# Kernel tuning notes

Measured on AMD Instinct MI355X. Metric: run time of the kernel, lower is better.

Reference implementation:

```python
import jax, jax.numpy as jnp
import numpy as np

# fixed-point config (matches init_kwargs)
DIM, H = 768, 12
DHEAD = DIM // H
DATA_W, DATA_F = 32, 16        # input activation quantizer
WQ = WK = WV = WP = (16, 8)    # weight quantizers (width, frac)
BQ = BK = BV = BP = (16, 8)    # bias quantizers
DQ = DK = DV = DS = DZ = (16, 8)  # activation quantizers after each stage
OUT_W, OUT_F = 32, 8


def qfix(x, width, frac):
    """Fixed-point integer quantizer: round to 2^-frac grid, clamp to signed width."""
    scale = jnp.float32(2.0 ** frac)
    lo = -(2.0 ** (width - 1))
    hi = 2.0 ** (width - 1) - 1
    return jnp.clip(jnp.round(x * scale), lo, hi) / scale


def setup_inputs() -> dict:
    key = jax.random.key(0)
    ks = jax.random.split(key, 5)
    return {
        "q_in": jax.random.normal(ks[0], (2, 2048, DIM), dtype=jnp.float32),
        "wqkv": jax.random.normal(ks[1], (3 * DIM, DIM), dtype=jnp.float32) * 0.05,
        "bqkv": jax.random.normal(ks[2], (3 * DIM,), dtype=jnp.float32) * 0.05,
        "wp": jax.random.normal(ks[3], (DIM, DIM), dtype=jnp.float32) * 0.05,
        "bp": jax.random.normal(ks[4], (DIM,), dtype=jnp.float32) * 0.05,
    }


def reference(q_in, wqkv, bqkv, wp, bp):
    B, N, _ = q_in.shape
    # per-head weight split: wqkv -> (H, 3*DHEAD, DIM), rows [0:d]=q, [d:2d]=k, [2d:3d]=v
    w = wqkv.reshape(H, 3 * DHEAD, DIM)
    b = bqkv.reshape(H, 3 * DHEAD)
    wq_, wk_, wv_ = w[:, :DHEAD], w[:, DHEAD:2 * DHEAD], w[:, 2 * DHEAD:]
    bq_, bk_, bv_ = b[:, :DHEAD], b[:, DHEAD:2 * DHEAD], b[:, 2 * DHEAD:]

    x = qfix(q_in, DATA_W, DATA_F)  # QuantizedLinear input quantization

    def qlin(wt, bt, wcfg, bcfg, ocfg):
        # y[b,h,n,e] = x[b,n,d] @ qw[h,e,d]^T + qb[h,e], then output quantize
        y = jnp.einsum('bnd,hed->bhne', x, qfix(wt, *wcfg)) + qfix(bt, *bcfg)[None, :, None, :]
        return qfix(y, *ocfg)

    q = qlin(wq_, bq_, WQ, BQ, DQ)  # (B,H,N,DHEAD)
    k = qlin(wk_, bk_, WK, BK, DK)
    v = qlin(wv_, bv_, WV, BV, DV)

    s = qfix(jnp.einsum('bhne,bhme->bhnm', q, k), *DS)   # (B,H,N,N) quantized scores
    z = qfix(jnp.einsum('bhnm,bhme->bhne', s, v), *DZ)   # (B,H,N,DHEAD)

    # concat heads along feature dim (torch.cat dim=2)
    zc = z.transpose(0, 2, 1, 3).reshape(B, N, DIM)

    # quantized projection: input quantized with data_z cfg (idempotent here)
    out = jnp.einsum('bnd,ed->bne', qfix(zc, *DZ), qfix(wp, *WP)) + qfix(bp, *BP)
    return qfix(out, OUT_W, OUT_F)
```

## Files before the change

### kernel.cpp

```cpp
#include <hip/hip_runtime.h>


#define NTOK 4096
#define DIM  768
#define NH   12
#define DH   64
#define SEQ  2048
#define QKVD 2304
#define NBH  24
#define LSTR 72

typedef _Float16 half8 __attribute__((ext_vector_type(8)));
typedef _Float16 half4 __attribute__((ext_vector_type(4)));
typedef __fp16   fp16x2 __attribute__((ext_vector_type(2)));
typedef float floatx4 __attribute__((ext_vector_type(4)));
typedef float floatx16 __attribute__((ext_vector_type(16)));

__global__ __launch_bounds__(256) void prep(
    const float* __restrict__ X,
    const float* __restrict__ wqkv, const float* __restrict__ bqkv,
    const float* __restrict__ wp,   const float* __restrict__ bp,
    _Float16* __restrict__ Xh, _Float16* __restrict__ Xl,
    _Float16* __restrict__ W16, _Float16* __restrict__ Wp16,
    float* __restrict__ bq24, float* __restrict__ bp16)
{
    int i = blockIdx.x * 256 + threadIdx.x;
    int i4 = i * 4;
    if (i4 < NTOK * DIM) {
        float4 x = *(const float4*)(X + i4);
        float xi[4] = {x.x, x.y, x.z, x.w};
        half4 oh, ol;
#pragma unroll
        for (int j = 0; j < 4; ++j) {
            float v = rintf(xi[j] * 65536.0f);
            float h = rintf(v * (1.0f / 2048.0f));
            ((_Float16*)&oh)[j] = (_Float16)h;
            ((_Float16*)&ol)[j] = (_Float16)(v - 2048.0f * h);
        }
        *(half4*)(Xh + i4) = oh;
        *(half4*)(Xl + i4) = ol;
    }
    if (i4 < QKVD * DIM) {
        float4 w = *(const float4*)(wqkv + i4);
        half4 o = {(_Float16)rintf(w.x * 256.0f), (_Float16)rintf(w.y * 256.0f),
                   (_Float16)rintf(w.z * 256.0f), (_Float16)rintf(w.w * 256.0f)};
        *(half4*)(W16 + i4) = o;
    }
    if (i4 < DIM * DIM) {
        float4 w = *(const float4*)(wp + i4);
        half4 o = {(_Float16)rintf(w.x * 256.0f), (_Float16)rintf(w.y * 256.0f),
                   (_Float16)rintf(w.z * 256.0f), (_Float16)rintf(w.w * 256.0f)};
        *(half4*)(Wp16 + i4) = o;
    }
    if (i < QKVD) bq24[i] = rintf(bqkv[i] * 256.0f) * 65536.0f;
    if (i < DIM)  bp16[i] = rintf(bp[i] * 256.0f) * 256.0f;
}

__global__ __launch_bounds__(256) void qkv_mfma(
    const _Float16* __restrict__ Xh, const _Float16* __restrict__ Xl,
    const _Float16* __restrict__ W16, const float* __restrict__ bq24,
    _Float16* __restrict__ Q16, _Float16* __restrict__ K16,
    _Float16* __restrict__ Vt16)
{
    __shared__ __align__(16) _Float16 Ah[64 * LSTR];
    __shared__ __align__(16) _Float16 Al[64 * LSTR];
    __shared__ __align__(16) _Float16 Bs[128 * LSTR];
    const int t = threadIdx.x;
    const int wave = t >> 6, lane = t & 63;
    const int lrow = lane & 15, quad = lane >> 4;
    const int m0 = blockIdx.y * 64;
    const int col0 = blockIdx.x * 128;

    floatx4 acch[4][2], accl[4][2];
#pragma unroll
    for (int fm = 0; fm < 4; ++fm)
#pragma unroll
        for (int fn = 0; fn < 2; ++fn) {
            acch[fm][fn] = (floatx4){0.f, 0.f, 0.f, 0.f};
            accl[fm][fn] = (floatx4){0.f, 0.f, 0.f, 0.f};
        }

    for (int k0 = 0; k0 < DIM; k0 += 64) {
        __syncthreads();
#pragma unroll
        for (int i = 0; i < 2; ++i) {
            int id = t + 256 * i;
            int r = id >> 3, c8 = id & 7;
            *(half8*)(&Ah[r * LSTR + c8 * 8]) =
                *(const half8*)(Xh + (size_t)(m0 + r) * DIM + k0 + c8 * 8);
            *(half8*)(&Al[r * LSTR + c8 * 8]) =
                *(const half8*)(Xl + (size_t)(m0 + r) * DIM + k0 + c8 * 8);
        }
#pragma unroll
        for (int i = 0; i < 4; ++i) {
            int id = t + 256 * i;
            int r = id >> 3, c8 = id & 7;
            *(half8*)(&Bs[r * LSTR + c8 * 8]) =
                *(const half8*)(W16 + (size_t)(col0 + r) * DIM + k0 + c8 * 8);
        }
        __syncthreads();
#pragma unroll
        for (int kk = 0; kk < 64; kk += 32) {
            half8 bf[2];
#pragma unroll
            for (int fn = 0; fn < 2; ++fn)
                bf[fn] = *(const half8*)(&Bs[(wave * 32 + fn * 16 + lrow) * LSTR + kk + quad * 8]);
#pragma unroll
            for (int fm = 0; fm < 4; ++fm) {
                half8 ah = *(const half8*)(&Ah[(fm * 16 + lrow) * LSTR + kk + quad * 8]);
                half8 al = *(const half8*)(&Al[(fm * 16 + lrow) * LSTR + kk + quad * 8]);
#pragma unroll
                for (int fn = 0; fn < 2; ++fn) {
                    acch[fm][fn] = __builtin_amdgcn_mfma_f32_16x16x32_f16(ah, bf[fn], acch[fm][fn], 0, 0, 0);
                    accl[fm][fn] = __builtin_amdgcn_mfma_f32_16x16x32_f16(al, bf[fn], accl[fm][fn], 0, 0, 0);
                }
            }
        }
    }

    const int b_ = m0 >> 11;
    const int n0base = m0 & 2047;
#pragma unroll
    for (int fn = 0; fn < 2; ++fn) {
        const int c = col0 + wave * 32 + fn * 16 + lrow;
        const int h = c / 192;
        const int jj = c % 192;
        const int kind = jj >> 6;
        const int e = jj & 63;
        const int bh = b_ * NH + h;
        const float bb = bq24[c];
#pragma unroll
        for (int fm = 0; fm < 4; ++fm) {
            float qv[4];
#pragma unroll
            for (int rg = 0; rg < 4; ++rg) {
                float y = fmaf(2048.0f, acch[fm][fn][rg], accl[fm][fn][rg]) + bb;
                float q = rintf(y * (1.0f / 65536.0f));
                qv[rg] = fminf(fmaxf(q, -32768.0f), 32767.0f);
            }
            if (kind == 2) {
                const int n0v = n0base + fm * 16 + 8 * (quad & 1) + 4 * (quad >> 1);
                half4 o = {(_Float16)qv[0], (_Float16)qv[1], (_Float16)qv[2], (_Float16)qv[3]};
                *(half4*)(Vt16 + ((size_t)bh * DH + e) * SEQ + n0v) = o;
            } else {
                const int n0 = n0base + fm * 16 + quad * 4;
                _Float16* dst = (kind == 0) ? Q16 : K16;
#pragma unroll
                for (int rg = 0; rg < 4; ++rg)
                    dst[((size_t)bh * SEQ + n0 + rg) * DH + e] = (_Float16)qv[rg];
            }
        }
    }
}

__global__ __launch_bounds__(256, 3) void attention_mfma(
    const _Float16* __restrict__ Q16, const _Float16* __restrict__ K16,
    const _Float16* __restrict__ Vt16,
    _Float16* __restrict__ Zh16, _Float16* __restrict__ Zl16)
{
    __shared__ __align__(16) char smem[64 * LSTR * 2 * 2];
    _Float16* Ks = (_Float16*)smem;
    _Float16* Vs = Ks + 64 * LSTR;
    float* scr = (float*)smem;

    const int t = threadIdx.x;
    const int bh = blockIdx.x;
    const int qt = blockIdx.y;
    const int w = t >> 6, lane = t & 63;
    const int l31 = lane & 31, hi = lane >> 5;
    const int wj = w & 1;
    const int wi = w >> 1;
    const _Float16* Qg = Q16 + ((size_t)bh * SEQ + qt * 64) * DH;
    const _Float16* Kg = K16 + (size_t)bh * SEQ * DH;
    const _Float16* Vg = Vt16 + (size_t)bh * DH * SEQ;

    half8 qf[4];
#pragma unroll
    for (int i = 0; i < 4; ++i)
        qf[i] = *(const half8*)(Qg + (32 * wj + l31) * DH + 16 * i + 8 * hi);

    floatx16 acc0h, acc0l, acc1h, acc1l;
#pragma unroll
    for (int r = 0; r < 16; ++r) { acc0h[r] = 0.f; acc0l[r] = 0.f; acc1h[r] = 0.f; acc1l[r] = 0.f; }

    for (int m0 = 0; m0 < SEQ; m0 += 64) {
        __syncthreads();
        {
            int r = t >> 3, k8 = t & 7;
            *(half8*)(&Ks[r * LSTR + k8 * 8]) =
                *(const half8*)(Kg + (size_t)(m0 + r) * DH + k8 * 8);
            *(half8*)(&Vs[r * LSTR + k8 * 8]) =
                *(const half8*)(Vg + (size_t)r * SEQ + m0 + k8 * 8);
            int t2 = t + 256; int r2 = t2 >> 3, k82 = t2 & 7;
            *(half8*)(&Ks[r2 * LSTR + k82 * 8]) =
                *(const half8*)(Kg + (size_t)(m0 + r2) * DH + k82 * 8);
            *(half8*)(&Vs[r2 * LSTR + k82 * 8]) =
                *(const half8*)(Vg + (size_t)r2 * SEQ + m0 + k82 * 8);
        }
        __syncthreads();

        floatx16 sc;
#pragma unroll
        for (int r = 0; r < 16; ++r) sc[r] = 0.f;
#pragma unroll
        for (int i = 0; i < 4; ++i) {
            half8 kf = *(const half8*)(&Ks[(32 * wi + l31) * LSTR + 16 * i + 8 * hi]);
            sc = __builtin_amdgcn_mfma_f32_32x32x16_f16(kf, qf[i], sc, 0, 0, 0);
        }

        float hh[16], ll[16];
#pragma unroll
        for (int r = 0; r < 16; ++r) {
            float v = rintf(sc[r] * 0.00390625f);
            v = fminf(fmaxf(v, -32768.0f), 32767.0f);
            float h = rintf(v * (1.0f / 2048.0f));
            hh[r] = h;
            ll[r] = fmaf(-2048.0f, h, v);
        }
        int dwh[4][2], dwl[4][2];
        union { fp16x2 h; int i; } cv;
#pragma unroll
        for (int g = 0; g < 4; ++g) {
            cv.h = __builtin_amdgcn_cvt_pkrtz(hh[4 * g + 0], hh[4 * g + 1]); dwh[g][0] = cv.i;
            cv.h = __builtin_amdgcn_cvt_pkrtz(hh[4 * g + 2], hh[4 * g + 3]); dwh[g][1] = cv.i;
            cv.h = __builtin_amdgcn_cvt_pkrtz(ll[4 * g + 0], ll[4 * g + 1]); dwl[g][0] = cv.i;
            cv.h = __builtin_amdgcn_cvt_pkrtz(ll[4 * g + 2], ll[4 * g + 3]); dwl[g][1] = cv.i;
        }

        half8 vf[2][2];
#pragma unroll
        for (int et = 0; et < 2; ++et)
#pragma unroll
            for (int c = 0; c < 2; ++c)
                vf[et][c] = *(const half8*)(&Vs[(32 * et + l31) * LSTR + 32 * wi + 16 * c + 8 * hi]);
#pragma unroll
        for (int c = 0; c < 2; ++c) {
            union { int b[4]; half8 v; } ubh, ubl;
            ubh.b[0] = dwh[2 * c][0];     ubh.b[1] = dwh[2 * c][1];
            ubh.b[2] = dwh[2 * c + 1][0]; ubh.b[3] = dwh[2 * c + 1][1];
            ubl.b[0] = dwl[2 * c][0];     ubl.b[1] = dwl[2 * c][1];
            ubl.b[2] = dwl[2 * c + 1][0]; ubl.b[3] = dwl[2 * c + 1][1];
            acc0h = __builtin_amdgcn_mfma_f32_32x32x16_f16(vf[0][c], ubh.v, acc0h, 0, 0, 0);
            acc0l = __builtin_amdgcn_mfma_f32_32x32x16_f16(vf[0][c], ubl.v, acc0l, 0, 0, 0);
            acc1h = __builtin_amdgcn_mfma_f32_32x32x16_f16(vf[1][c], ubh.v, acc1h, 0, 0, 0);
            acc1l = __builtin_amdgcn_mfma_f32_32x32x16_f16(vf[1][c], ubl.v, acc1l, 0, 0, 0);
        }
    }

    float zfh[16], zfl[16];
    {
        __syncthreads();
#pragma unroll
        for (int r = 0; r < 16; ++r) {
            int er = (r & 3) + 8 * (r >> 2) + 4 * hi;
            float sendh = wi ? acc0h[r] : acc1h[r];
            scr[((wj * 2 + (1 - wi)) * 32 + er) * 33 + l31] = sendh;
        }
        __syncthreads();
#pragma unroll
        for (int r = 0; r < 16; ++r) {
            int er = (r & 3) + 8 * (r >> 2) + 4 * hi;
            float keeph = wi ? acc1h[r] : acc0h[r];
            zfh[r] = keeph + scr[((wj * 2 + wi) * 32 + er) * 33 + l31];
        }
        __syncthreads();
#pragma unroll
        for (int r = 0; r < 16; ++r) {
            int er = (r & 3) + 8 * (r >> 2) + 4 * hi;
            float sendl = wi ? acc0l[r] : acc1l[r];
            scr[((wj * 2 + (1 - wi)) * 32 + er) * 33 + l31] = sendl;
        }
        __syncthreads();
#pragma unroll
        for (int r = 0; r < 16; ++r) {
            int er = (r & 3) + 8 * (r >> 2) + 4 * hi;
            float keepl = wi ? acc1l[r] : acc0l[r];
            zfl[r] = keepl + scr[((wj * 2 + wi) * 32 + er) * 33 + l31];
        }
    }

    const int b_ = bh / NH, h = bh % NH;
    const int n = qt * 64 + 32 * wj + l31;
    const size_t rowoff = ((size_t)b_ * SEQ + n) * DIM + h * DH;
#pragma unroll
    for (int g = 0; g < 4; ++g) {
        int e0 = 32 * wi + 8 * g + 4 * hi;
        half4 ph, pl;
#pragma unroll
        for (int j = 0; j < 4; ++j) {
            int r = 4 * g + j;
            float zint = fmaf(2048.0f, zfh[r], zfl[r]);
            float zq = rintf(zint * 0.00390625f);
            zq = fminf(fmaxf(zq, -32768.0f), 32767.0f);
            float zdh = rintf(zq * (1.0f / 2048.0f));
            ((_Float16*)&ph)[j] = (_Float16)zdh;
            ((_Float16*)&pl)[j] = (_Float16)(zq - 2048.0f * zdh);
        }
        *(half4*)(Zh16 + rowoff + e0) = ph;
        *(half4*)(Zl16 + rowoff + e0) = pl;
    }
}

__global__ __launch_bounds__(256) void out_mfma(
    const _Float16* __restrict__ Zh, const _Float16* __restrict__ Zl,
    const _Float16* __restrict__ Wp16, const float* __restrict__ bp16,
    float* __restrict__ O)
{
    __shared__ __align__(16) _Float16 Ah[64 * LSTR];
    __shared__ __align__(16) _Float16 Al[64 * LSTR];
    __shared__ __align__(16) _Float16 Bs[128 * LSTR];
    const int t = threadIdx.x;
    const int wave = t >> 6, lane = t & 63;
    const int lrow = lane & 15, quad = lane >> 4;
    const int m0 = blockIdx.y * 64;
    const int col0 = blockIdx.x * 128;

    floatx4 acch[4][2], accl[4][2];
#pragma unroll
    for (int fm = 0; fm < 4; ++fm)
#pragma unroll
        for (int fn = 0; fn < 2; ++fn) {
            acch[fm][fn] = (floatx4){0.f, 0.f, 0.f, 0.f};
            accl[fm][fn] = (floatx4){0.f, 0.f, 0.f, 0.f};
        }

    for (int k0 = 0; k0 < DIM; k0 += 64) {
        __syncthreads();
#pragma unroll
        for (int i = 0; i < 2; ++i) {
            int id = t + 256 * i;
            int r = id >> 3, c8 = id & 7;
            *(half8*)(&Ah[r * LSTR + c8 * 8]) =
                *(const half8*)(Zh + (size_t)(m0 + r) * DIM + k0 + c8 * 8);
            *(half8*)(&Al[r * LSTR + c8 * 8]) =
                *(const half8*)(Zl + (size_t)(m0 + r) * DIM + k0 + c8 * 8);
        }
#pragma unroll
        for (int i = 0; i < 4; ++i) {
            int id = t + 256 * i;
            int r = id >> 3, c8 = id & 7;
            *(half8*)(&Bs[r * LSTR + c8 * 8]) =
                *(const half8*)(Wp16 + (size_t)(col0 + r) * DIM + k0 + c8 * 8);
        }
        __syncthreads();
#pragma unroll
        for (int kk = 0; kk < 64; kk += 32) {
            half8 bf[2];
#pragma unroll
            for (int fn = 0; fn < 2; ++fn)
                bf[fn] = *(const half8*)(&Bs[(wave * 32 + fn * 16 + lrow) * LSTR + kk + quad * 8]);
#pragma unroll
            for (int fm = 0; fm < 4; ++fm) {
                half8 ah = *(const half8*)(&Ah[(fm * 16 + lrow) * LSTR + kk + quad * 8]);
                half8 al = *(const half8*)(&Al[(fm * 16 + lrow) * LSTR + kk + quad * 8]);
#pragma unroll
                for (int fn = 0; fn < 2; ++fn) {
                    acch[fm][fn] = __builtin_amdgcn_mfma_f32_16x16x32_f16(ah, bf[fn], acch[fm][fn], 0, 0, 0);
                    accl[fm][fn] = __builtin_amdgcn_mfma_f32_16x16x32_f16(al, bf[fn], accl[fm][fn], 0, 0, 0);
                }
            }
        }
    }

#pragma unroll
    for (int fn = 0; fn < 2; ++fn) {
        const int c = col0 + wave * 32 + fn * 16 + lrow;
        const float bb = bp16[c];
#pragma unroll
        for (int fm = 0; fm < 4; ++fm)
#pragma unroll
            for (int rg = 0; rg < 4; ++rg) {
                float y = fmaf(2048.0f, acch[fm][fn][rg], accl[fm][fn][rg]) + bb;
                float o = rintf(y * 0.00390625f) * 0.00390625f;
                int r = m0 + fm * 16 + quad * 4 + rg;
                O[(size_t)r * DIM + c] = o;
            }
    }
}

extern "C" void kernel_launch(void* const* d_in, const int* in_sizes, int n_in,
                              void* d_out, int out_size, void* d_ws, size_t ws_size,
                              hipStream_t stream) {
    const float* q_in = (const float*)d_in[0];
    const float* wqkv = (const float*)d_in[1];
    const float* bqkv = (const float*)d_in[2];
    const float* wp   = (const float*)d_in[3];
    const float* bp   = (const float*)d_in[4];

    char* w = (char*)d_ws;
    _Float16* W16  = (_Float16*)w;  w += (size_t)QKVD * DIM * 2;
    _Float16* Wp16 = (_Float16*)w;  w += (size_t)DIM * DIM * 2;
    float* bq24    = (float*)w;     w += QKVD * 4;
    float* bp16    = (float*)w;     w += DIM * 4;
    _Float16* Xh   = (_Float16*)w;  w += (size_t)NTOK * DIM * 2;
    _Float16* Xl   = (_Float16*)w;  w += (size_t)NTOK * DIM * 2;
    _Float16* Q16  = (_Float16*)w;  w += (size_t)NBH * SEQ * DH * 2;
    _Float16* K16  = (_Float16*)w;  w += (size_t)NBH * SEQ * DH * 2;
    _Float16* Vt16 = (_Float16*)w;  w += (size_t)NBH * SEQ * DH * 2;
    _Float16* Zh16 = (_Float16*)w;  w += (size_t)NTOK * DIM * 2;
    _Float16* Zl16 = (_Float16*)w;  w += (size_t)NTOK * DIM * 2;
    (void)ws_size; (void)in_sizes; (void)n_in; (void)out_size;

    prep<<<dim3(NTOK * DIM / 4 / 256), 256, 0, stream>>>(
        q_in, wqkv, bqkv, wp, bp, Xh, Xl, W16, Wp16, bq24, bp16);
    qkv_mfma<<<dim3(QKVD / 128, NTOK / 64), 256, 0, stream>>>(
        Xh, Xl, W16, bq24, Q16, K16, Vt16);
    attention_mfma<<<dim3(NBH, SEQ / 64), 256, 0, stream>>>(Q16, K16, Vt16, Zh16, Zl16);
    out_mfma<<<dim3(DIM / 128, NTOK / 64), 256, 0, stream>>>(
        Zh16, Zl16, Wp16, bp16, (float*)d_out);
}
```

Measured before the change: 189.9 us.

## Retile QKV GEMM to 128x128 blocks with 32x32x16 MFMA

Rewrites the QKV projection kernel to compute a 128x128 output tile per block, where each wave owns 32 rows across four 32-column tiles, using the 32x32x16 f16 MFMA instead of 16x16x32. This raises arithmetic intensity per LDS load and halves the number of blocks. The grid order is swapped so M tiles vary fastest, which changes L2 reuse of the weight tiles. The larger accumulators (128 fp32 per lane) raise register pressure, and launch bounds are set to two blocks per CU.

New measurement: 184.9 us. -2.7%, faster.

```diff
diff --git a/kernel.cpp b/kernel.cpp
--- a/kernel.cpp
+++ b/kernel.cpp
@@ -56,98 +56,86 @@
     if (i < DIM)  bp16[i] = rintf(bp[i] * 256.0f) * 256.0f;
 }
 
-__global__ __launch_bounds__(256) void qkv_mfma(
+__global__ __launch_bounds__(256, 2) void qkv_mfma(
     const _Float16* __restrict__ Xh, const _Float16* __restrict__ Xl,
     const _Float16* __restrict__ W16, const float* __restrict__ bq24,
     _Float16* __restrict__ Q16, _Float16* __restrict__ K16,
     _Float16* __restrict__ Vt16)
 {
-    __shared__ __align__(16) _Float16 Ah[64 * LSTR];
-    __shared__ __align__(16) _Float16 Al[64 * LSTR];
+    __shared__ __align__(16) _Float16 Ah[128 * LSTR];
+    __shared__ __align__(16) _Float16 Al[128 * LSTR];
     __shared__ __align__(16) _Float16 Bs[128 * LSTR];
     const int t = threadIdx.x;
-    const int wave = t >> 6, lane = t & 63;
-    const int lrow = lane & 15, quad = lane >> 4;
-    const int m0 = blockIdx.y * 64;
-    const int col0 = blockIdx.x * 128;
-
-    floatx4 acch[4][2], accl[4][2];
-#pragma unroll
-    for (int fm = 0; fm < 4; ++fm)
-#pragma unroll
-        for (int fn = 0; fn < 2; ++fn) {
-            acch[fm][fn] = (floatx4){0.f, 0.f, 0.f, 0.f};
-            accl[fm][fn] = (floatx4){0.f, 0.f, 0.f, 0.f};
-        }
+    const int w = t >> 6, lane = t & 63;
+    const int l31 = lane & 31, hi = lane >> 5;
+    const int m0 = blockIdx.x * 128;
+    const int col0 = blockIdx.y * 128;
+
+    floatx16 acch[4], accl[4];
+#pragma unroll
+    for (int ct = 0; ct < 4; ++ct)
+#pragma unroll
+        for (int r = 0; r < 16; ++r) { acch[ct][r] = 0.f; accl[ct][r] = 0.f; }
 
     for (int k0 = 0; k0 < DIM; k0 += 64) {
         __syncthreads();
 #pragma unroll
-        for (int i = 0; i < 2; ++i) {
+        for (int i = 0; i < 4; ++i) {
             int id = t + 256 * i;
             int r = id >> 3, c8 = id & 7;
             *(half8*)(&Ah[r * LSTR + c8 * 8]) =
                 *(const half8*)(Xh + (size_t)(m0 + r) * DIM + k0 + c8 * 8);
             *(half8*)(&Al[r * LSTR + c8 * 8]) =
                 *(const half8*)(Xl + (size_t)(m0 + r) * DIM + k0 + c8 * 8);
-        }
-#pragma unroll
-        for (int i = 0; i < 4; ++i) {
-            int id = t + 256 * i;
-            int r = id >> 3, c8 = id & 7;
             *(half8*)(&Bs[r * LSTR + c8 * 8]) =
                 *(const half8*)(W16 + (size_t)(col0 + r) * DIM + k0 + c8 * 8);
         }
         __syncthreads();
 #pragma unroll
-        for (int kk = 0; kk < 64; kk += 32) {
-            half8 bf[2];
-#pragma unroll
-            for (int fn = 0; fn < 2; ++fn)
-                bf[fn] = *(const half8*)(&Bs[(wave * 32 + fn * 16 + lrow) * LSTR + kk + quad * 8]);
-#pragma unroll
-            for (int fm = 0; fm < 4; ++fm) {
-                half8 ah = *(const half8*)(&Ah[(fm * 16 + lrow) * LSTR + kk + quad * 8]);
-                half8 al = *(const half8*)(&Al[(fm * 16 + lrow) * LSTR + kk + quad * 8]);
-#pragma unroll
-                for (int fn = 0; fn < 2; ++fn) {
-                    acch[fm][fn] = __builtin_amdgcn_mfma_f32_16x16x32_f16(ah, bf[fn], acch[fm][fn], 0, 0, 0);
-                    accl[fm][fn] = __builtin_amdgcn_mfma_f32_16x16x32_f16(al, bf[fn], accl[fm][fn], 0, 0, 0);
-                }
+        for (int i = 0; i < 4; ++i) {
+            half8 ah = *(const half8*)(&Ah[(32 * w + l31) * LSTR + 16 * i + 8 * hi]);
+            half8 al = *(const half8*)(&Al[(32 * w + l31) * LSTR + 16 * i + 8 * hi]);
+#pragma unroll
+            for (int ct = 0; ct < 4; ++ct) {
+                half8 bf = *(const half8*)(&Bs[(32 * ct + l31) * LSTR + 16 * i + 8 * hi]);
+                acch[ct] = __builtin_amdgcn_mfma_f32_32x32x16_f16(ah, bf, acch[ct], 0, 0, 0);
+                accl[ct] = __builtin_amdgcn_mfma_f32_32x32x16_f16(al, bf, accl[ct], 0, 0, 0);
             }
         }
     }
 
     const int b_ = m0 >> 11;
-    const int n0base = m0 & 2047;
-#pragma unroll
-    for (int fn = 0; fn < 2; ++fn) {
-        const int c = col0 + wave * 32 + fn * 16 + lrow;
+    const int nbase = (m0 & 2047) + 32 * w;
+#pragma unroll
+    for (int ct = 0; ct < 4; ++ct) {
+        const int c = col0 + 32 * ct + l31;
         const int h = c / 192;
         const int jj = c % 192;
         const int kind = jj >> 6;
         const int e = jj & 63;
         const int bh = b_ * NH + h;
         const float bb = bq24[c];
-#pragma unroll
-        for (int fm = 0; fm < 4; ++fm) {
-            float qv[4];
-#pragma unroll
-            for (int rg = 0; rg < 4; ++rg) {
-                float y = fmaf(2048.0f, acch[fm][fn][rg], accl[fm][fn][rg]) + bb;
-                float q = rintf(y * (1.0f / 65536.0f));
-                qv[rg] = fminf(fmaxf(q, -32768.0f), 32767.0f);
-            }
-            if (kind == 2) {
-                const int n0v = n0base + fm * 16 + 8 * (quad & 1) + 4 * (quad >> 1);
-                half4 o = {(_Float16)qv[0], (_Float16)qv[1], (_Float16)qv[2], (_Float16)qv[3]};
-                *(half4*)(Vt16 + ((size_t)bh * DH + e) * SEQ + n0v) = o;
-            } else {
-                const int n0 = n0base + fm * 16 + quad * 4;
-                _Float16* dst = (kind == 0) ? Q16 : K16;
-#pragma unroll
-                for (int rg = 0; rg < 4; ++rg)
-                    dst[((size_t)bh * SEQ + n0 + rg) * DH + e] = (_Float16)qv[rg];
+        float qv[16];
+#pragma unroll
+        for (int r = 0; r < 16; ++r) {
+            float y = fmaf(2048.0f, acch[ct][r], accl[ct][r]) + bb;
+            float q = rintf(y * (1.0f / 65536.0f));
+            qv[r] = fminf(fmaxf(q, -32768.0f), 32767.0f);
+        }
+        if (kind == 2) {
+#pragma unroll
+            for (int g = 0; g < 4; ++g) {
+                int nv = nbase + 16 * (g >> 1) + 8 * hi + 4 * (g & 1);
+                half4 o = {(_Float16)qv[4 * g + 0], (_Float16)qv[4 * g + 1],
+                           (_Float16)qv[4 * g + 2], (_Float16)qv[4 * g + 3]};
+                *(half4*)(Vt16 + ((size_t)bh * DH + e) * SEQ + nv) = o;
+            }
+        } else {
+            _Float16* dst = (kind == 0) ? Q16 : K16;
+#pragma unroll
+            for (int r = 0; r < 16; ++r) {
+                int er = (r & 3) + 8 * (r >> 2) + 4 * hi;
+                dst[((size_t)bh * SEQ + nbase + er) * DH + e] = (_Float16)qv[r];
             }
         }
     }
@@ -403,7 +391,7 @@
 
     prep<<<dim3(NTOK * DIM / 4 / 256), 256, 0, stream>>>(
         q_in, wqkv, bqkv, wp, bp, Xh, Xl, W16, Wp16, bq24, bp16);
-    qkv_mfma<<<dim3(QKVD / 128, NTOK / 64), 256, 0, stream>>>(
+    qkv_mfma<<<dim3(NTOK / 128, QKVD / 128), 256, 0, stream>>>(
         Xh, Xl, W16, bq24, Q16, K16, Vt16);
     attention_mfma<<<dim3(NBH, SEQ / 64), 256, 0, stream>>>(Q16, K16, Vt16, Zh16, Zl16);
     out_mfma<<<dim3(DIM / 128, NTOK / 64), 256, 0, stream>>>(
```
